# Performance work log

Measured on AMD Instinct MI355X. Metric: run time of the kernel, lower is better.

## Reference

```python
import jax, jax.numpy as jnp
import numpy as np

EMBED = 128          # embed_dim
HID = 128            # hidden_dim (must equal embed_dim for the view math to work)
HEADS = 4
HEAD_DIM = EMBED // HEADS  # = HID // HEADS = 32
N = 50000            # source cells
M = 50000            # target cells
E = 400000           # edges (nnz of inter_neighborhood)


def setup_inputs() -> dict:
    key = jax.random.key(0)
    ks = jax.random.split(key, 13)
    s = lambda d: 1.0 / np.sqrt(d)
    return {
        "source_features": jax.random.normal(ks[0], (N, EMBED), jnp.float32),
        "target_features": jax.random.normal(ks[1], (M, EMBED), jnp.float32),
        "edge_targets": jax.random.randint(ks[2], (E,), 0, M, dtype=jnp.int32),
        "edge_sources": jax.random.randint(ks[3], (E,), 0, N, dtype=jnp.int32),
        "Ws": jax.random.normal(ks[4], (EMBED, HEADS * HID), jnp.float32) * s(EMBED),
        "bs": jnp.zeros((HEADS * HID,), jnp.float32),
        "Wt": jax.random.normal(ks[5], (EMBED, HEADS * HID), jnp.float32) * s(EMBED),
        "bt": jnp.zeros((HEADS * HID,), jnp.float32),
        "attn_w": jax.random.normal(ks[6], (HEADS, HID), jnp.float32),
        "Wm": jax.random.normal(ks[7], (EMBED, EMBED), jnp.float32) * s(EMBED),
        "bm": jnp.zeros((EMBED,), jnp.float32),
        "Wo": jax.random.normal(ks[8], (EMBED, EMBED), jnp.float32) * s(EMBED),
        "bo": jnp.zeros((EMBED,), jnp.float32),
    }


def reference(source_features, target_features, edge_targets, edge_sources,
              Ws, bs, Wt, bt, attn_w, Wm, bm, Wo, bo):
    # Gather endpoint features per edge: [E, EMBED]
    src = source_features[edge_sources]
    tgt = target_features[edge_targets]
    # Fused linear + GELU attention hidden: [E, HEADS, HID]
    hidden = jax.nn.gelu((src @ Ws + bs) + (tgt @ Wt + bt), approximate=False)
    hidden = hidden.reshape(E, HEADS, HID)
    # Attention logits per edge/head: [E, HEADS]
    logits = jnp.einsum('ehd,hd->eh', hidden, attn_w)
    # Scatter-softmax over edges sharing the same target node
    mx = jax.ops.segment_max(logits, edge_targets, num_segments=M)
    ex = jnp.exp(logits - mx[edge_targets])
    den = jax.ops.segment_sum(ex, edge_targets, num_segments=M)
    scores = ex / den[edge_targets]                      # [E, HEADS]
    # Messages: [E, HEADS, HEAD_DIM], weighted and scatter-summed to targets
    msgs = (src @ Wm + bm).reshape(E, HEADS, HEAD_DIM) * scores[..., None]
    agg = jax.ops.segment_sum(msgs, edge_targets, num_segments=M)
    agg = agg.reshape(M, HEADS * HEAD_DIM)               # [M, EMBED]
    return agg @ Wo + bo
```

## Files before the change

### kernel.cpp

```cpp
#include <hip/hip_runtime.h>
#include <math.h>


typedef __bf16 bf16x8 __attribute__((ext_vector_type(8)));
typedef float  f32x4  __attribute__((ext_vector_type(4)));
typedef float  f32x2  __attribute__((ext_vector_type(2)));

__device__ __forceinline__ unsigned short f2bf(float x) {
    unsigned u = __float_as_uint(x);
    u += 0x7FFFu + ((u >> 16) & 1u);
    return (unsigned short)(u >> 16);
}
__device__ __forceinline__ float bf2f(unsigned short b) {
    return __uint_as_float(((unsigned)b) << 16);
}
__device__ __forceinline__ f32x2 up2(unsigned u) {
    f32x2 r;
    r.x = __uint_as_float(u << 16);
    r.y = __uint_as_float(u & 0xFFFF0000u);
    return r;
}
__device__ __forceinline__ float exp2_fast(float x) {
#if __has_builtin(__builtin_amdgcn_exp2f)
    return __builtin_amdgcn_exp2f(x);
#else
    return exp2f(x);
#endif
}

__device__ __forceinline__ f32x2 gelu2(f32x2 v) {
    f32x2 v2 = v * v;
    f32x2 u  = v * (v2 * 0.10294355f + 2.30220820f);
    f32x2 e;
    e.x = exp2_fast(u.x);
    e.y = exp2_fast(u.y);
    f32x2 r;
    r.x = __builtin_amdgcn_rcpf(e.x + 1.0f);
    r.y = __builtin_amdgcn_rcpf(e.y + 1.0f);
    return v - v * r;
}

__device__ __forceinline__ float edge_logit(uint4 h,
    f32x2 ht0, f32x2 ht1, f32x2 ht2, f32x2 ht3,
    f32x2 aw0, f32x2 aw1, f32x2 aw2, f32x2 aw3) {
    f32x2 qv = gelu2(up2(h.x) + ht0) * aw0;
    qv += gelu2(up2(h.y) + ht1) * aw1;
    qv += gelu2(up2(h.z) + ht2) * aw2;
    qv += gelu2(up2(h.w) + ht3) * aw3;
    return qv.x + qv.y;
}

__global__ __launch_bounds__(256)
void cast_split_kernel(const float* __restrict__ src, const float* __restrict__ tgt,
                       unsigned short* __restrict__ shi, unsigned short* __restrict__ slo,
                       unsigned short* __restrict__ thi, unsigned short* __restrict__ tlo,
                       int n4src, int n4tot) {
    int i = blockIdx.x * blockDim.x + threadIdx.x;
    if (i >= n4tot) return;
    const float* in; unsigned short *hi, *lo; int j;
    if (i < n4src) { in = src; hi = shi; lo = slo; j = i; }
    else           { in = tgt; hi = thi; lo = tlo; j = i - n4src; }
    float4 v = *(const float4*)(in + (size_t)j * 4);
    ushort4 h, l;
    h.x = f2bf(v.x); l.x = f2bf(v.x - bf2f(h.x));
    h.y = f2bf(v.y); l.y = f2bf(v.y - bf2f(h.y));
    h.z = f2bf(v.z); l.z = f2bf(v.z - bf2f(h.z));
    h.w = f2bf(v.w); l.w = f2bf(v.w - bf2f(h.w));
    *(ushort4*)(hi + (size_t)j * 4) = h;
    *(ushort4*)(lo + (size_t)j * 4) = l;
}

__global__ __launch_bounds__(128)
void prep_weights_kernel(const float* __restrict__ Ws, const float* __restrict__ Wm,
                         const float* __restrict__ Wt, const float* __restrict__ Wo,
                         const float* __restrict__ bs, const float* __restrict__ bm,
                         unsigned short* __restrict__ WThi, unsigned short* __restrict__ WTlo,
                         float* __restrict__ bias_cat) {
    int n = blockIdx.x, k = threadIdx.x;
    float w;
    if      (n < 512)  w = Ws[(size_t)k * 512 + n];
    else if (n < 640)  w = Wm[(size_t)k * 128 + (n - 512)];
    else if (n < 1152) w = Wt[(size_t)k * 512 + (n - 640)];
    else               w = Wo[(size_t)k * 128 + (n - 1152)];
    unsigned short hi = f2bf(w);
    WThi[(size_t)n * 128 + k] = hi;
    WTlo[(size_t)n * 128 + k] = f2bf(w - bf2f(hi));
    if (k == 0 && n < 640) bias_cat[n] = (n < 512) ? bs[n] : bm[n - 512];
}

__global__ void hist_kernel(const int* __restrict__ tgt, int* __restrict__ counts, int E) {
    int e = blockIdx.x * blockDim.x + threadIdx.x;
    if (e < E) atomicAdd(&counts[tgt[e]], 1);
}

__global__ __launch_bounds__(256)
void scan_partial_kernel(const int* __restrict__ counts, int* __restrict__ partials, int M) {
    __shared__ int sdata[256];
    int b = blockIdx.x, tid = threadIdx.x;
    int base = b * 1024 + tid * 4;
    int s = 0;
#pragma unroll
    for (int k = 0; k < 4; ++k) { int idx = base + k; if (idx < M) s += counts[idx]; }
    sdata[tid] = s; __syncthreads();
    for (int d = 128; d > 0; d >>= 1) {
        if (tid < d) sdata[tid] += sdata[tid + d];
        __syncthreads();
    }
    if (tid == 0) partials[b] = sdata[0];
}

__global__ __launch_bounds__(64)
void scan_partials_kernel(const int* __restrict__ partials, int* __restrict__ pbase,
                          int* __restrict__ offsets, int P, int M) {
    int lane = threadIdx.x;
    int own = (lane < P) ? partials[lane] : 0;
    int v = own;
    for (int d = 1; d < 64; d <<= 1) {
        int o = __shfl_up(v, d);
        if (lane >= d) v += o;
    }
    if (lane < P) pbase[lane] = v - own;
    if (lane == 63) offsets[M] = v;
}

__global__ __launch_bounds__(256)
void scan_final_kernel(const int* __restrict__ counts, const int* __restrict__ pbase,
                       int* __restrict__ offsets, int M) {
    __shared__ int sdata[256];
    int b = blockIdx.x, tid = threadIdx.x;
    int base = b * 1024 + tid * 4;
    int c0 = 0, c1 = 0, c2 = 0, c3 = 0;
    if (base + 0 < M) c0 = counts[base + 0];
    if (base + 1 < M) c1 = counts[base + 1];
    if (base + 2 < M) c2 = counts[base + 2];
    if (base + 3 < M) c3 = counts[base + 3];
    int s = c0 + c1 + c2 + c3;
    sdata[tid] = s; __syncthreads();
    int v = s;
    for (int d = 1; d < 256; d <<= 1) {
        int o = (tid >= d) ? sdata[tid - d] : 0;
        __syncthreads();
        v += o;
        sdata[tid] = v;
        __syncthreads();
    }
    int ex = pbase[b] + v - s;
    if (base + 0 < M) offsets[base + 0] = ex;
    if (base + 1 < M) offsets[base + 1] = ex + c0;
    if (base + 2 < M) offsets[base + 2] = ex + c0 + c1;
    if (base + 3 < M) offsets[base + 3] = ex + c0 + c1 + c2;
}

__global__ void scatter_kernel(const int* __restrict__ tgt, const int* __restrict__ src,
                               const int* __restrict__ offsets,
                               int* __restrict__ cursor, int* __restrict__ srcs_sorted, int E) {
    int e = blockIdx.x * blockDim.x + threadIdx.x;
    if (e < E) {
        int t = tgt[e];
        int r = atomicAdd(&cursor[t], 1);
        srcs_sorted[offsets[t] + r] = src[e];
    }
}

__global__ __launch_bounds__(256, 4)
void gemm_hidden_kernel(const unsigned short* __restrict__ shi, const unsigned short* __restrict__ slo,
                        const unsigned short* __restrict__ thi, const unsigned short* __restrict__ tlo,
                        const unsigned short* __restrict__ WThi, const unsigned short* __restrict__ WTlo,
                        const float* __restrict__ bias_cat, const float* __restrict__ bt,
                        unsigned short* __restrict__ Hs, unsigned short* __restrict__ Hm,
                        unsigned short* __restrict__ Ht, int N, int M) {
    __shared__ unsigned short Ahi[64 * 72], Alo[64 * 72];
    __shared__ unsigned short Bhi[64 * 72], Blo[64 * 72];

    int i = blockIdx.x;
    int x = i & 7;
    int k = i >> 3;
    int cb = k % 18;
    int rg = k / 18;
    int row_tile = rg * 8 + x;

    bool side1 = cb >= 10;
    const unsigned short* Ahi_g = side1 ? thi : shi;
    const unsigned short* Alo_g = side1 ? tlo : slo;
    int rows = side1 ? M : N;
    int row0 = row_tile * 64;
    if (row0 >= rows) return;
    int colL = side1 ? (cb - 10) * 64 : cb * 64;
    int colW = side1 ? 640 + colL : colL;
    const float* bias = side1 ? bt : bias_cat;

    int tid = threadIdx.x;
    int wid = tid >> 6, lane = tid & 63;
    int wm = (wid >> 1) * 32, wn = (wid & 1) * 32;
    int g = lane >> 4, r16 = lane & 15;

    f32x4 acc00 = {0.f, 0.f, 0.f, 0.f}, acc01 = acc00, acc10 = acc00, acc11 = acc00;

    for (int kb = 0; kb < 128; kb += 64) {
#pragma unroll
        for (int l = 0; l < 2; ++l) {
            int idx = l * 256 + tid;
            int r = idx >> 3, c8 = idx & 7;
            int row = row0 + r;
            uint4 vh = make_uint4(0, 0, 0, 0), vl = vh;
            if (row < rows) {
                vh = *(const uint4*)(Ahi_g + (size_t)row * 128 + kb + c8 * 8);
                vl = *(const uint4*)(Alo_g + (size_t)row * 128 + kb + c8 * 8);
            }
            *(uint4*)(&Ahi[r * 72 + c8 * 8]) = vh;
            *(uint4*)(&Alo[r * 72 + c8 * 8]) = vl;
            uint4 wh = *(const uint4*)(WThi + (size_t)(colW + r) * 128 + kb + c8 * 8);
            uint4 wl = *(const uint4*)(WTlo + (size_t)(colW + r) * 128 + kb + c8 * 8);
            *(uint4*)(&Bhi[r * 72 + c8 * 8]) = wh;
            *(uint4*)(&Blo[r * 72 + c8 * 8]) = wl;
        }
        __syncthreads();

#pragma unroll
        for (int kk = 0; kk < 2; ++kk) {
            int k0 = kk * 32 + g * 8;
            bf16x8 ah0 = *(const bf16x8*)(&Ahi[(wm + r16) * 72 + k0]);
            bf16x8 ah1 = *(const bf16x8*)(&Ahi[(wm + 16 + r16) * 72 + k0]);
            bf16x8 al0 = *(const bf16x8*)(&Alo[(wm + r16) * 72 + k0]);
            bf16x8 al1 = *(const bf16x8*)(&Alo[(wm + 16 + r16) * 72 + k0]);
            bf16x8 bh0 = *(const bf16x8*)(&Bhi[(wn + r16) * 72 + k0]);
            bf16x8 bh1 = *(const bf16x8*)(&Bhi[(wn + 16 + r16) * 72 + k0]);
            bf16x8 bl0 = *(const bf16x8*)(&Blo[(wn + r16) * 72 + k0]);
            bf16x8 bl1 = *(const bf16x8*)(&Blo[(wn + 16 + r16) * 72 + k0]);
            acc00 = __builtin_amdgcn_mfma_f32_16x16x32_bf16(ah0, bh0, acc00, 0, 0, 0);
            acc00 = __builtin_amdgcn_mfma_f32_16x16x32_bf16(ah0, bl0, acc00, 0, 0, 0);
            acc00 = __builtin_amdgcn_mfma_f32_16x16x32_bf16(al0, bh0, acc00, 0, 0, 0);
            acc01 = __builtin_amdgcn_mfma_f32_16x16x32_bf16(ah0, bh1, acc01, 0, 0, 0);
            acc01 = __builtin_amdgcn_mfma_f32_16x16x32_bf16(ah0, bl1, acc01, 0, 0, 0);
            acc01 = __builtin_amdgcn_mfma_f32_16x16x32_bf16(al0, bh1, acc01, 0, 0, 0);
            acc10 = __builtin_amdgcn_mfma_f32_16x16x32_bf16(ah1, bh0, acc10, 0, 0, 0);
            acc10 = __builtin_amdgcn_mfma_f32_16x16x32_bf16(ah1, bl0, acc10, 0, 0, 0);
            acc10 = __builtin_amdgcn_mfma_f32_16x16x32_bf16(al1, bh0, acc10, 0, 0, 0);
            acc11 = __builtin_amdgcn_mfma_f32_16x16x32_bf16(ah1, bh1, acc11, 0, 0, 0);
            acc11 = __builtin_amdgcn_mfma_f32_16x16x32_bf16(ah1, bl1, acc11, 0, 0, 0);
            acc11 = __builtin_amdgcn_mfma_f32_16x16x32_bf16(al1, bh1, acc11, 0, 0, 0);
        }
        __syncthreads();
    }

    int c0 = colL + wn + r16;
    int c1 = c0 + 16;
    float bv0 = bias[c0], bv1 = bias[c1];
#pragma unroll
    for (int ii = 0; ii < 4; ++ii) {
        int rA = row0 + wm + g * 4 + ii;
        int rB = rA + 16;
        if (rA < rows) {
            float o0 = acc00[ii] + bv0, o1 = acc01[ii] + bv1;
            if (side1) {
                Ht[(size_t)rA * 512 + c0] = f2bf(o0);
                Ht[(size_t)rA * 512 + c1] = f2bf(o1);
            } else {
                if (c0 < 512) Hs[(size_t)rA * 512 + c0] = f2bf(o0);
                else          Hm[(size_t)rA * 128 + (c0 - 512)] = f2bf(o0);
                if (c1 < 512) Hs[(size_t)rA * 512 + c1] = f2bf(o1);
                else          Hm[(size_t)rA * 128 + (c1 - 512)] = f2bf(o1);
            }
        }
        if (rB < rows) {
            float o0 = acc10[ii] + bv0, o1 = acc11[ii] + bv1;
            if (side1) {
                Ht[(size_t)rB * 512 + c0] = f2bf(o0);
                Ht[(size_t)rB * 512 + c1] = f2bf(o1);
            } else {
                if (c0 < 512) Hs[(size_t)rB * 512 + c0] = f2bf(o0);
                else          Hm[(size_t)rB * 128 + (c0 - 512)] = f2bf(o0);
                if (c1 < 512) Hs[(size_t)rB * 512 + c1] = f2bf(o1);
                else          Hm[(size_t)rB * 128 + (c1 - 512)] = f2bf(o1);
            }
        }
    }
}

__global__ __launch_bounds__(256, 4)
void gemm_out_kernel(const unsigned short* __restrict__ A,
                     const unsigned short* __restrict__ BT,
                     const float* __restrict__ bias,
                     float* __restrict__ C, int Mrows, int Ntot) {
    __shared__ unsigned short As[64 * 136];
    __shared__ unsigned short Bs[64 * 136];
    int tid = threadIdx.x;
    int row0 = blockIdx.y * 64, col0 = blockIdx.x * 64;

#pragma unroll
    for (int l = 0; l < 4; ++l) {
        int idx = l * 256 + tid;
        int r = idx >> 4, c8 = idx & 15;
        int row = row0 + r;
        uint4 v = make_uint4(0, 0, 0, 0);
        if (row < Mrows) v = *(const uint4*)(A + (size_t)row * 128 + c8 * 8);
        *(uint4*)(&As[r * 136 + c8 * 8]) = v;
    }
#pragma unroll
    for (int l = 0; l < 4; ++l) {
        int idx = l * 256 + tid;
        int r = idx >> 4, c8 = idx & 15;
        uint4 v = *(const uint4*)(BT + (size_t)(col0 + r) * 128 + c8 * 8);
        *(uint4*)(&Bs[r * 136 + c8 * 8]) = v;
    }
    __syncthreads();

    int wid = tid >> 6, lane = tid & 63;
    int wm = (wid >> 1) * 32, wn = (wid & 1) * 32;
    int g = lane >> 4, r16 = lane & 15;

    f32x4 acc00 = {0.f, 0.f, 0.f, 0.f}, acc01 = acc00, acc10 = acc00, acc11 = acc00;

#pragma unroll
    for (int kk = 0; kk < 4; ++kk) {
        int k0 = kk * 32 + g * 8;
        bf16x8 a0 = *(const bf16x8*)(&As[(wm + r16) * 136 + k0]);
        bf16x8 a1 = *(const bf16x8*)(&As[(wm + 16 + r16) * 136 + k0]);
        bf16x8 b0 = *(const bf16x8*)(&Bs[(wn + r16) * 136 + k0]);
        bf16x8 b1 = *(const bf16x8*)(&Bs[(wn + 16 + r16) * 136 + k0]);
        acc00 = __builtin_amdgcn_mfma_f32_16x16x32_bf16(a0, b0, acc00, 0, 0, 0);
        acc01 = __builtin_amdgcn_mfma_f32_16x16x32_bf16(a0, b1, acc01, 0, 0, 0);
        acc10 = __builtin_amdgcn_mfma_f32_16x16x32_bf16(a1, b0, acc10, 0, 0, 0);
        acc11 = __builtin_amdgcn_mfma_f32_16x16x32_bf16(a1, b1, acc11, 0, 0, 0);
    }

    float bv0 = bias[col0 + wn + r16];
    float bv1 = bias[col0 + wn + 16 + r16];
#pragma unroll
    for (int i = 0; i < 4; ++i) {
        int rA = row0 + wm + g * 4 + i;
        int rB = rA + 16;
        if (rA < Mrows) {
            C[(size_t)rA * Ntot + col0 + wn + r16]      = acc00[i] + bv0;
            C[(size_t)rA * Ntot + col0 + wn + 16 + r16] = acc01[i] + bv1;
        }
        if (rB < Mrows) {
            C[(size_t)rB * Ntot + col0 + wn + r16]      = acc10[i] + bv0;
            C[(size_t)rB * Ntot + col0 + wn + 16 + r16] = acc11[i] + bv1;
        }
    }
}

__global__ __launch_bounds__(256)
void attn_kernel(const unsigned short* __restrict__ Hs, const unsigned short* __restrict__ Ht,
                 const unsigned short* __restrict__ Hm, const float* __restrict__ attn_w,
                 const int* __restrict__ offsets, const int* __restrict__ srcs,
                 unsigned short* __restrict__ agg, int M) {
    int wave = threadIdx.x >> 6;
    int lane = threadIdx.x & 63;
    int t = blockIdx.x * 4 + wave;
    if (t >= M) return;

    int j0 = lane << 3;
    uint4 h = *(const uint4*)(Ht + (size_t)t * 512 + j0);
    f32x2 ht0 = up2(h.x), ht1 = up2(h.y), ht2 = up2(h.z), ht3 = up2(h.w);
    const float L2E = 1.4426950408889634f;
    float4 a0 = *(const float4*)(attn_w + j0);
    float4 a1 = *(const float4*)(attn_w + j0 + 4);
    f32x2 aw0 = {a0.x * L2E, a0.y * L2E};
    f32x2 aw1 = {a0.z * L2E, a0.w * L2E};
    f32x2 aw2 = {a1.x * L2E, a1.y * L2E};
    f32x2 aw3 = {a1.z * L2E, a1.w * L2E};

    int off = offsets[t];
    int end = offsets[t + 1];

    float m = -INFINITY, den = 0.f;
    f32x2 acc = {0.f, 0.f};
    int hm_off = lane << 1;

    int i = off;
    for (; i + 3 < end; i += 4) {
        int s0 = srcs[i], s1 = srcs[i + 1], s2 = srcs[i + 2], s3 = srcs[i + 3];
        uint4 hA = *(const uint4*)(Hs + (size_t)s0 * 512 + j0);
        uint4 hB = *(const uint4*)(Hs + (size_t)s1 * 512 + j0);
        uint4 hC = *(const uint4*)(Hs + (size_t)s2 * 512 + j0);
        uint4 hD = *(const uint4*)(Hs + (size_t)s3 * 512 + j0);
        unsigned mA = *(const unsigned*)(Hm + (size_t)s0 * 128 + hm_off);
        unsigned mB = *(const unsigned*)(Hm + (size_t)s1 * 128 + hm_off);
        unsigned mC = *(const unsigned*)(Hm + (size_t)s2 * 128 + hm_off);
        unsigned mD = *(const unsigned*)(Hm + (size_t)s3 * 128 + hm_off);
        float q0 = edge_logit(hA, ht0, ht1, ht2, ht3, aw0, aw1, aw2, aw3);
        float q1 = edge_logit(hB, ht0, ht1, ht2, ht3, aw0, aw1, aw2, aw3);
        float q2 = edge_logit(hC, ht0, ht1, ht2, ht3, aw0, aw1, aw2, aw3);
        float q3 = edge_logit(hD, ht0, ht1, ht2, ht3, aw0, aw1, aw2, aw3);
        q0 += __shfl_xor(q0, 1); q1 += __shfl_xor(q1, 1); q2 += __shfl_xor(q2, 1); q3 += __shfl_xor(q3, 1);
        q0 += __shfl_xor(q0, 2); q1 += __shfl_xor(q1, 2); q2 += __shfl_xor(q2, 2); q3 += __shfl_xor(q3, 2);
        q0 += __shfl_xor(q0, 4); q1 += __shfl_xor(q1, 4); q2 += __shfl_xor(q2, 4); q3 += __shfl_xor(q3, 4);
        q0 += __shfl_xor(q0, 8); q1 += __shfl_xor(q1, 8); q2 += __shfl_xor(q2, 8); q3 += __shfl_xor(q3, 8);

        float nm = fmaxf(fmaxf(fmaxf(q0, q1), fmaxf(q2, q3)), m);
        float sc = exp2_fast(m - nm);
        float p0 = exp2_fast(q0 - nm);
        float p1 = exp2_fast(q1 - nm);
        float p2 = exp2_fast(q2 - nm);
        float p3 = exp2_fast(q3 - nm);
        den = fmaf(den, sc, (p0 + p1) + (p2 + p3));
        acc = acc * sc;
        acc += p0 * up2(mA);
        acc += p1 * up2(mB);
        acc += p2 * up2(mC);
        acc += p3 * up2(mD);
        m = nm;
    }
    for (; i < end; ++i) {
        int s0 = srcs[i];
        uint4 hA = *(const uint4*)(Hs + (size_t)s0 * 512 + j0);
        unsigned mA = *(const unsigned*)(Hm + (size_t)s0 * 128 + hm_off);
        float q0 = edge_logit(hA, ht0, ht1, ht2, ht3, aw0, aw1, aw2, aw3);
        q0 += __shfl_xor(q0, 1);
        q0 += __shfl_xor(q0, 2);
        q0 += __shfl_xor(q0, 4);
        q0 += __shfl_xor(q0, 8);
        float nm = fmaxf(m, q0);
        float sc = exp2_fast(m - nm);
        float p0 = exp2_fast(q0 - nm);
        den = fmaf(den, sc, p0);
        acc = acc * sc + p0 * up2(mA);
        m = nm;
    }
    float r = (end > off) ? __builtin_amdgcn_rcpf(den) : 0.0f;
    ushort2 o;
    o.x = f2bf(acc.x * r);
    o.y = f2bf(acc.y * r);
    *(ushort2*)(agg + (size_t)t * 128 + hm_off) = o;
}

extern "C" void kernel_launch(void* const* d_in, const int* in_sizes, int n_in,
                              void* d_out, int out_size, void* d_ws, size_t ws_size,
                              hipStream_t stream) {
    const float* src_f  = (const float*)d_in[0];
    const float* tgt_f  = (const float*)d_in[1];
    const int*   e_tgt  = (const int*)d_in[2];
    const int*   e_src  = (const int*)d_in[3];
    const float* Ws     = (const float*)d_in[4];
    const float* bs     = (const float*)d_in[5];
    const float* Wt     = (const float*)d_in[6];
    const float* bt     = (const float*)d_in[7];
    const float* attn_w = (const float*)d_in[8];
    const float* Wm     = (const float*)d_in[9];
    const float* bm     = (const float*)d_in[10];
    const float* Wo     = (const float*)d_in[11];
    const float* bo     = (const float*)d_in[12];

    int N = in_sizes[0] / 128;
    int M = in_sizes[1] / 128;
    int E = in_sizes[2];

    char* ws = (char*)d_ws;
    size_t woff = 0;
    auto alloc = [&](size_t bytes) -> void* {
        void* p = ws + woff;
        woff += ((bytes + 255) / 256) * 256;
        return p;
    };
    unsigned short* Hs       = (unsigned short*)alloc((size_t)N * 512 * 2);
    unsigned short* Ht       = (unsigned short*)alloc((size_t)M * 512 * 2);
    unsigned short* Hm       = (unsigned short*)alloc((size_t)N * 128 * 2);
    unsigned short* agg_bf   = (unsigned short*)alloc((size_t)M * 128 * 2);
    unsigned short* shi      = (unsigned short*)alloc((size_t)N * 128 * 2);
    unsigned short* slo      = (unsigned short*)alloc((size_t)N * 128 * 2);
    unsigned short* thi      = (unsigned short*)alloc((size_t)M * 128 * 2);
    unsigned short* tlo      = (unsigned short*)alloc((size_t)M * 128 * 2);
    unsigned short* WThi     = (unsigned short*)alloc((size_t)1280 * 128 * 2);
    unsigned short* WTlo     = (unsigned short*)alloc((size_t)1280 * 128 * 2);
    float*          bias_cat = (float*)alloc(640 * 4);
    int*            counts   = (int*)alloc((size_t)M * 4);
    int*            cursor   = (int*)alloc((size_t)M * 4);
    int*            offsets  = (int*)alloc((size_t)(M + 1) * 4);
    int*            srcs     = (int*)alloc((size_t)E * 4);
    int*            partials = (int*)alloc(64 * 4);
    int*            pbase    = (int*)alloc(64 * 4);

    hipMemsetAsync(counts, 0, (size_t)M * 4, stream);
    hipMemsetAsync(cursor, 0, (size_t)M * 4, stream);

    const int tb = 256;
    int P = (M + 1023) / 1024;

    hist_kernel<<<(E + tb - 1) / tb, tb, 0, stream>>>(e_tgt, counts, E);
    scan_partial_kernel<<<P, 256, 0, stream>>>(counts, partials, M);
    scan_partials_kernel<<<1, 64, 0, stream>>>(partials, pbase, offsets, P, M);
    scan_final_kernel<<<P, 256, 0, stream>>>(counts, pbase, offsets, M);
    scatter_kernel<<<(E + tb - 1) / tb, tb, 0, stream>>>(e_tgt, e_src, offsets, cursor, srcs, E);

    int n4src = N * 32, n4tot = (N + M) * 32;
    cast_split_kernel<<<(n4tot + tb - 1) / tb, tb, 0, stream>>>(src_f, tgt_f, shi, slo, thi, tlo,
                                                               n4src, n4tot);
    prep_weights_kernel<<<1280, 128, 0, stream>>>(Ws, Wm, Wt, Wo, bs, bm, WThi, WTlo, bias_cat);

    int rowsMax = (N > M) ? N : M;
    int nRowTiles = (rowsMax + 63) / 64;
    int nRG = (nRowTiles + 7) / 8;
    gemm_hidden_kernel<<<8 * 18 * nRG, 256, 0, stream>>>(shi, slo, thi, tlo, WThi, WTlo,
                                                         bias_cat, bt, Hs, Hm, Ht, N, M);

    attn_kernel<<<(M + 3) / 4, 256, 0, stream>>>(Hs, Ht, Hm, attn_w, offsets, srcs, agg_bf, M);

    dim3 go(128 / 64, (M + 63) / 64);
    gemm_out_kernel<<<go, 256, 0, stream>>>(agg_bf, WThi + (size_t)1152 * 128, bo,
                                            (float*)d_out, M, 128);
}
```

Measured before the change: 357.5 us.

## Fuse fp32 hi/lo bf16 split into hidden GEMM and prefetch edges in attention

Removes the separate cast_split kernel and its intermediate hi/lo buffers; the hidden GEMM now loads fp32 source/target rows directly and splits them into bf16 hi/lo while staging into shared memory. The attention loop is software-pipelined to issue the next batch of four gathered Hs/Hm loads before computing the current batch. The two counter memsets are merged into one. This saves a full read/write pass over the features and a launch, at the cost of repeated conversion work per column block and higher register use in the attention kernel.

```diff
diff --git a/kernel.cpp b/kernel.cpp
--- a/kernel.cpp
+++ b/kernel.cpp
@@ -48,26 +48,6 @@
     qv += gelu2(up2(h.z) + ht2) * aw2;
     qv += gelu2(up2(h.w) + ht3) * aw3;
     return qv.x + qv.y;
-}
-
-__global__ __launch_bounds__(256)
-void cast_split_kernel(const float* __restrict__ src, const float* __restrict__ tgt,
-                       unsigned short* __restrict__ shi, unsigned short* __restrict__ slo,
-                       unsigned short* __restrict__ thi, unsigned short* __restrict__ tlo,
-                       int n4src, int n4tot) {
-    int i = blockIdx.x * blockDim.x + threadIdx.x;
-    if (i >= n4tot) return;
-    const float* in; unsigned short *hi, *lo; int j;
-    if (i < n4src) { in = src; hi = shi; lo = slo; j = i; }
-    else           { in = tgt; hi = thi; lo = tlo; j = i - n4src; }
-    float4 v = *(const float4*)(in + (size_t)j * 4);
-    ushort4 h, l;
-    h.x = f2bf(v.x); l.x = f2bf(v.x - bf2f(h.x));
-    h.y = f2bf(v.y); l.y = f2bf(v.y - bf2f(h.y));
-    h.z = f2bf(v.z); l.z = f2bf(v.z - bf2f(h.z));
-    h.w = f2bf(v.w); l.w = f2bf(v.w - bf2f(h.w));
-    *(ushort4*)(hi + (size_t)j * 4) = h;
-    *(ushort4*)(lo + (size_t)j * 4) = l;
 }
 
 __global__ __launch_bounds__(128)
@@ -163,8 +143,7 @@
 }
 
 __global__ __launch_bounds__(256, 4)
-void gemm_hidden_kernel(const unsigned short* __restrict__ shi, const unsigned short* __restrict__ slo,
-                        const unsigned short* __restrict__ thi, const unsigned short* __restrict__ tlo,
+void gemm_hidden_kernel(const float* __restrict__ src_f, const float* __restrict__ tgt_f,
                         const unsigned short* __restrict__ WThi, const unsigned short* __restrict__ WTlo,
                         const float* __restrict__ bias_cat, const float* __restrict__ bt,
                         unsigned short* __restrict__ Hs, unsigned short* __restrict__ Hm,
@@ -180,8 +159,7 @@
     int row_tile = rg * 8 + x;
 
     bool side1 = cb >= 10;
-    const unsigned short* Ahi_g = side1 ? thi : shi;
-    const unsigned short* Alo_g = side1 ? tlo : slo;
+    const float* Af = side1 ? tgt_f : src_f;
     int rows = side1 ? M : N;
     int row0 = row_tile * 64;
     if (row0 >= rows) return;
@@ -202,13 +180,24 @@
             int idx = l * 256 + tid;
             int r = idx >> 3, c8 = idx & 7;
             int row = row0 + r;
-            uint4 vh = make_uint4(0, 0, 0, 0), vl = vh;
+            float4 v0 = make_float4(0.f, 0.f, 0.f, 0.f), v1 = v0;
             if (row < rows) {
-                vh = *(const uint4*)(Ahi_g + (size_t)row * 128 + kb + c8 * 8);
-                vl = *(const uint4*)(Alo_g + (size_t)row * 128 + kb + c8 * 8);
+                v0 = *(const float4*)(Af + (size_t)row * 128 + kb + c8 * 8);
+                v1 = *(const float4*)(Af + (size_t)row * 128 + kb + c8 * 8 + 4);
             }
-            *(uint4*)(&Ahi[r * 72 + c8 * 8]) = vh;
-            *(uint4*)(&Alo[r * 72 + c8 * 8]) = vl;
+            ushort4 h0, h1, o0, o1;
+            h0.x = f2bf(v0.x); o0.x = f2bf(v0.x - bf2f(h0.x));
+            h0.y = f2bf(v0.y); o0.y = f2bf(v0.y - bf2f(h0.y));
+            h0.z = f2bf(v0.z); o0.z = f2bf(v0.z - bf2f(h0.z));
+            h0.w = f2bf(v0.w); o0.w = f2bf(v0.w - bf2f(h0.w));
+            h1.x = f2bf(v1.x); o1.x = f2bf(v1.x - bf2f(h1.x));
+            h1.y = f2bf(v1.y); o1.y = f2bf(v1.y - bf2f(h1.y));
+            h1.z = f2bf(v1.z); o1.z = f2bf(v1.z - bf2f(h1.z));
+            h1.w = f2bf(v1.w); o1.w = f2bf(v1.w - bf2f(h1.w));
+            *(ushort4*)(&Ahi[r * 72 + c8 * 8])     = h0;
+            *(ushort4*)(&Ahi[r * 72 + c8 * 8 + 4]) = h1;
+            *(ushort4*)(&Alo[r * 72 + c8 * 8])     = o0;
+            *(ushort4*)(&Alo[r * 72 + c8 * 8 + 4]) = o1;
             uint4 wh = *(const uint4*)(WThi + (size_t)(colW + r) * 128 + kb + c8 * 8);
             uint4 wl = *(const uint4*)(WTlo + (size_t)(colW + r) * 128 + kb + c8 * 8);
             *(uint4*)(&Bhi[r * 72 + c8 * 8]) = wh;
@@ -364,22 +353,43 @@
 
     int off = offsets[t];
     int end = offsets[t + 1];
+    int hm_off = lane << 1;
 
     float m = -INFINITY, den = 0.f;
     f32x2 acc = {0.f, 0.f};
-    int hm_off = lane << 1;
 
     int i = off;
-    for (; i + 3 < end; i += 4) {
+    uint4 hA, hB, hC, hD;
+    unsigned mA, mB, mC, mD;
+    bool have = (end - i) >= 4;
+    if (have) {
         int s0 = srcs[i], s1 = srcs[i + 1], s2 = srcs[i + 2], s3 = srcs[i + 3];
-        uint4 hA = *(const uint4*)(Hs + (size_t)s0 * 512 + j0);
-        uint4 hB = *(const uint4*)(Hs + (size_t)s1 * 512 + j0);
-        uint4 hC = *(const uint4*)(Hs + (size_t)s2 * 512 + j0);
-        uint4 hD = *(const uint4*)(Hs + (size_t)s3 * 512 + j0);
-        unsigned mA = *(const unsigned*)(Hm + (size_t)s0 * 128 + hm_off);
-        unsigned mB = *(const unsigned*)(Hm + (size_t)s1 * 128 + hm_off);
-        unsigned mC = *(const unsigned*)(Hm + (size_t)s2 * 128 + hm_off);
-        unsigned mD = *(const unsigned*)(Hm + (size_t)s3 * 128 + hm_off);
+        hA = *(const uint4*)(Hs + (size_t)s0 * 512 + j0);
+        hB = *(const uint4*)(Hs + (size_t)s1 * 512 + j0);
+        hC = *(const uint4*)(Hs + (size_t)s2 * 512 + j0);
+        hD = *(const uint4*)(Hs + (size_t)s3 * 512 + j0);
+        mA = *(const unsigned*)(Hm + (size_t)s0 * 128 + hm_off);
+        mB = *(const unsigned*)(Hm + (size_t)s1 * 128 + hm_off);
+        mC = *(const unsigned*)(Hm + (size_t)s2 * 128 + hm_off);
+        mD = *(const unsigned*)(Hm + (size_t)s3 * 128 + hm_off);
+    }
+    while (have) {
+        int ni = i + 4;
+        bool nhave = (end - ni) >= 4;
+        uint4 nhA, nhB, nhC, nhD;
+        unsigned nmA, nmB, nmC, nmD;
+        if (nhave) {
+            int s0 = srcs[ni], s1 = srcs[ni + 1], s2 = srcs[ni + 2], s3 = srcs[ni + 3];
+            nhA = *(const uint4*)(Hs + (size_t)s0 * 512 + j0);
+            nhB = *(const uint4*)(Hs + (size_t)s1 * 512 + j0);
+            nhC = *(const uint4*)(Hs + (size_t)s2 * 512 + j0);
+            nhD = *(const uint4*)(Hs + (size_t)s3 * 512 + j0);
+            nmA = *(const unsigned*)(Hm + (size_t)s0 * 128 + hm_off);
+            nmB = *(const unsigned*)(Hm + (size_t)s1 * 128 + hm_off);
+            nmC = *(const unsigned*)(Hm + (size_t)s2 * 128 + hm_off);
+            nmD = *(const unsigned*)(Hm + (size_t)s3 * 128 + hm_off);
+        }
+
         float q0 = edge_logit(hA, ht0, ht1, ht2, ht3, aw0, aw1, aw2, aw3);
         float q1 = edge_logit(hB, ht0, ht1, ht2, ht3, aw0, aw1, aw2, aw3);
         float q2 = edge_logit(hC, ht0, ht1, ht2, ht3, aw0, aw1, aw2, aw3);
@@ -402,12 +412,19 @@
         acc += p2 * up2(mC);
         acc += p3 * up2(mD);
         m = nm;
+
+        i = ni;
+        if (nhave) {
+            hA = nhA; hB = nhB; hC = nhC; hD = nhD;
+            mA = nmA; mB = nmB; mC = nmC; mD = nmD;
+        }
+        have = nhave;
     }
     for (; i < end; ++i) {
         int s0 = srcs[i];
-        uint4 hA = *(const uint4*)(Hs + (size_t)s0 * 512 + j0);
-        unsigned mA = *(const unsigned*)(Hm + (size_t)s0 * 128 + hm_off);
-        float q0 = edge_logit(hA, ht0, ht1, ht2, ht3, aw0, aw1, aw2, aw3);
+        uint4 hX = *(const uint4*)(Hs + (size_t)s0 * 512 + j0);
+        unsigned mX = *(const unsigned*)(Hm + (size_t)s0 * 128 + hm_off);
+        float q0 = edge_logit(hX, ht0, ht1, ht2, ht3, aw0, aw1, aw2, aw3);
         q0 += __shfl_xor(q0, 1);
         q0 += __shfl_xor(q0, 2);
         q0 += __shfl_xor(q0, 4);
@@ -416,7 +433,7 @@
         float sc = exp2_fast(m - nm);
         float p0 = exp2_fast(q0 - nm);
         den = fmaf(den, sc, p0);
-        acc = acc * sc + p0 * up2(mA);
+        acc = acc * sc + p0 * up2(mX);
         m = nm;
     }
     float r = (end > off) ? __builtin_amdgcn_rcpf(den) : 0.0f;
@@ -458,22 +475,17 @@
     unsigned short* Ht       = (unsigned short*)alloc((size_t)M * 512 * 2);
     unsigned short* Hm       = (unsigned short*)alloc((size_t)N * 128 * 2);
     unsigned short* agg_bf   = (unsigned short*)alloc((size_t)M * 128 * 2);
-    unsigned short* shi      = (unsigned short*)alloc((size_t)N * 128 * 2);
-    unsigned short* slo      = (unsigned short*)alloc((size_t)N * 128 * 2);
-    unsigned short* thi      = (unsigned short*)alloc((size_t)M * 128 * 2);
-    unsigned short* tlo      = (unsigned short*)alloc((size_t)M * 128 * 2);
     unsigned short* WThi     = (unsigned short*)alloc((size_t)1280 * 128 * 2);
     unsigned short* WTlo     = (unsigned short*)alloc((size_t)1280 * 128 * 2);
     float*          bias_cat = (float*)alloc(640 * 4);
-    int*            counts   = (int*)alloc((size_t)M * 4);
-    int*            cursor   = (int*)alloc((size_t)M * 4);
+    int*            counts   = (int*)alloc((size_t)2 * M * 4);
+    int*            cursor   = counts + M;
     int*            offsets  = (int*)alloc((size_t)(M + 1) * 4);
     int*            srcs     = (int*)alloc((size_t)E * 4);
     int*            partials = (int*)alloc(64 * 4);
     int*            pbase    = (int*)alloc(64 * 4);
 
-    hipMemsetAsync(counts, 0, (size_t)M * 4, stream);
-    hipMemsetAsync(cursor, 0, (size_t)M * 4, stream);
+    hipMemsetAsync(counts, 0, (size_t)2 * M * 4, stream);
 
     const int tb = 256;
     int P = (M + 1023) / 1024;
@@ -484,15 +496,12 @@
     scan_final_kernel<<<P, 256, 0, stream>>>(counts, pbase, offsets, M);
     scatter_kernel<<<(E + tb - 1) / tb, tb, 0, stream>>>(e_tgt, e_src, offsets, cursor, srcs, E);
 
-    int n4src = N * 32, n4tot = (N + M) * 32;
-    cast_split_kernel<<<(n4tot + tb - 1) / tb, tb, 0, stream>>>(src_f, tgt_f, shi, slo, thi, tlo,
-                                                               n4src, n4tot);
     prep_weights_kernel<<<1280, 128, 0, stream>>>(Ws, Wm, Wt, Wo, bs, bm, WThi, WTlo, bias_cat);
 
     int rowsMax = (N > M) ? N : M;
     int nRowTiles = (rowsMax + 63) / 64;
     int nRG = (nRowTiles + 7) / 8;
-    gemm_hidden_kernel<<<8 * 18 * nRG, 256, 0, stream>>>(shi, slo, thi, tlo, WThi, WTlo,
+    gemm_hidden_kernel<<<8 * 18 * nRG, 256, 0, stream>>>(src_f, tgt_f, WThi, WTlo,
                                                          bias_cat, bt, Hs, Hm, Ht, N, M);
 
     attn_kernel<<<(M + 3) / 4, 256, 0, stream>>>(Hs, Ht, Hm, attn_w, offsets, srcs, agg_bf, M);
```

After: 362.6 us. About the same (+1.4%).
